# Kernel tuning notes

Measured on AMD Instinct MI355X. Metric: run time of the kernel, lower is better.

The kernel has to match this reference:

```python
import jax, jax.numpy as jnp
import numpy as np

B, N, H = 8, 1024, 256
ALPHA = 0.25


def setup_inputs() -> dict:
    key = jax.random.key(0)
    ks = jax.random.split(key, 10)
    h_cat = jax.random.normal(ks[0], (B, N, H), jnp.float32) * 0.1
    # Random trees: every node j>=1 gets a parent p in [0, j-1], on the left or right side.
    rng = np.random.default_rng(0)
    parents = (rng.random((B, N)) * np.arange(N)).astype(np.int64)  # parents[b,0] unused
    side = rng.integers(0, 2, (B, N))
    left = np.zeros((B, N, N), np.float32)
    right = np.zeros((B, N, N), np.float32)
    bidx = np.repeat(np.arange(B), N - 1)
    jidx = np.tile(np.arange(1, N), B)
    pidx = parents[:, 1:].reshape(-1)
    sid = side[:, 1:].reshape(-1)
    l = sid == 0
    r = sid == 1
    left[bidx[l], pidx[l], jidx[l]] = 1.0
    right[bidx[r], pidx[r], jidx[r]] = 1.0
    roots = jnp.zeros((B,), jnp.int32)  # node 0 is the root of each random tree
    return {
        "h_cat": h_cat,
        "left_adj": jnp.asarray(left),
        "right_adj": jnp.asarray(right),
        "roots": roots,
        "W_bilin": jax.random.normal(ks[1], (2, H, H), jnp.float32) * 0.02,
        "b_bilin": jax.random.normal(ks[2], (2,), jnp.float32) * 0.02,
        "W_head": jax.random.normal(ks[3], (2, H), jnp.float32) * 0.1,
        "W_dep": jax.random.normal(ks[4], (2, H), jnp.float32) * 0.1,
        "W_r1": jax.random.normal(ks[5], (H, H), jnp.float32) * 0.05,
        "b_r1": jnp.zeros((H,), jnp.float32),
        "W_r2": jax.random.normal(ks[6], (1, H), jnp.float32) * 0.1,
        "b_r2": jnp.zeros((1,), jnp.float32),
    }


def reference(h_cat, left_adj, right_adj, roots, W_bilin, b_bilin, W_head, W_dep, W_r1, b_r1, W_r2, b_r2):
    b, n, _ = h_cat.shape
    # --- biaffine compat matrix [b,n,n,2] (get_compat_matrix / bilin_compat),
    # computed via einsum instead of materializing the repeat_interleave [b,n*n,H] tensors.
    tmp = jnp.einsum('bih,khg->bikg', h_cat, W_bilin)          # [b,n,2,H]
    bil = jnp.einsum('bikg,bjg->bijk', tmp, h_cat)              # [b,n,n,2]
    head = h_cat @ W_head.T                                     # [b,n,2]
    dep = h_cat @ W_dep.T                                       # [b,n,2]
    compat = bil + head[:, :, None, :] + dep[:, None, :, :] + b_bilin
    # --- root classifier: Linear -> GELU(exact) -> Linear, [b,n]
    root_scores = (jax.nn.gelu(h_cat @ W_r1.T + b_r1, approximate=False) @ W_r2.T + b_r2)[..., 0]
    # --- logistic_loss (matrix-tree theorem)
    gold = root_scores[jnp.arange(b), roots]
    gold = gold + jnp.sum(compat[..., 0] * left_adj, axis=(1, 2))
    gold = gold + jnp.sum(compat[..., 1] * right_adj, axis=(1, 2))
    A = jnp.sum(jnp.exp(compat), axis=3)                        # [b,n,n]
    colsum = jnp.sum(A, axis=1)                                 # [b,n]
    lap = -A
    diag = jnp.arange(n)
    lap = lap.at[:, diag, diag].add(colsum)                     # diag_embed(sum(A,1)) - A
    lap = lap.at[:, 0, :].set(jnp.exp(root_scores))             # replace row 0 with root potentials
    sign, logabs = jnp.linalg.slogdet(lap)
    logdet = jnp.where(sign > 0, logabs, jnp.nan)               # torch logdet -> nan for det<=0
    valid = ((~jnp.isnan(gold)) & (~jnp.isnan(logdet))).astype(gold.dtype)
    mask = (gold <= logdet * valid).astype(gold.dtype)
    loss = (logdet - gold) * mask
    loss = jnp.where(jnp.isnan(loss), 0.0, loss)
    return ALPHA * jnp.sum(loss) / b
```

## Files before the change

kernel.cpp:

```cpp
#include <hip/hip_runtime.h>
#include <math.h>

#define BB 8
#define NN 1024
#define HH 256
#define ALPHAC 0.25f

typedef short bf16x8 __attribute__((ext_vector_type(8)));
typedef unsigned short u16x8 __attribute__((ext_vector_type(8)));
typedef float f32x4 __attribute__((ext_vector_type(4)));

__device__ inline unsigned short f2bf(float x) {
  unsigned u = __builtin_bit_cast(unsigned, x);
  unsigned r = (u + 0x7fffu + ((u >> 16) & 1u)) >> 16;
  return (unsigned short)r;
}
__device__ inline float bf2f(unsigned short u) {
  return __builtin_bit_cast(float, (unsigned)u << 16);
}

__device__ inline int prm(int i) { return i == 0 ? 1023 : (i == 1023 ? 0 : i); }

static const size_t OFF_TMPBF = 0;
static const size_t OFF_HBF   = 2097152;
static const size_t OFF_BT    = 3145728;
static const size_t OFF_EL    = 3244040;
static const size_t OFF_EV    = 3252240;
static const size_t OFF_R1    = 3260448;
static const size_t OFF_M     = 4325376;
static const size_t OFF_SM    = 8519680;
static const size_t O_H0 = 0, O_H1 = 8192, O_D0 = 16384, O_D1 = 24576, O_RS = 32768;
static const size_t O_GOLD = 40960, O_SLOG = 40968, O_NEG = 40976, O_ZER = 40984;
static const size_t O_CS   = 40992;

__global__ __launch_bounds__(256) void kA_pre(const float* __restrict__ h_cat,
    const float* __restrict__ Wb, const float* __restrict__ Wr1,
    const float* __restrict__ W_head, const float* __restrict__ W_dep,
    const float* __restrict__ left, const float* __restrict__ right,
    unsigned short* __restrict__ h_bf, unsigned short* __restrict__ BT,
    float* __restrict__ head0, float* __restrict__ head1,
    float* __restrict__ dep0, float* __restrict__ dep1,
    unsigned* __restrict__ par) {
  int bid = blockIdx.x, tid = threadIdx.x;
  if (bid < 2048) {
    int wave = tid >> 6, lane = tid & 63;
    int row = bid * 4 + wave;
    float4 h4 = *(const float4*)&h_cat[(size_t)row * 256 + lane * 4];
    ushort4 o;
    o.x = f2bf(h4.x); o.y = f2bf(h4.y); o.z = f2bf(h4.z); o.w = f2bf(h4.w);
    *(ushort4*)&h_bf[(size_t)row * 256 + lane * 4] = o;
    float4 wh0 = *(const float4*)&W_head[lane * 4];
    float4 wh1 = *(const float4*)&W_head[256 + lane * 4];
    float4 wd0 = *(const float4*)&W_dep[lane * 4];
    float4 wd1 = *(const float4*)&W_dep[256 + lane * 4];
    float s0 = h4.x * wh0.x + h4.y * wh0.y + h4.z * wh0.z + h4.w * wh0.w;
    float s1 = h4.x * wh1.x + h4.y * wh1.y + h4.z * wh1.z + h4.w * wh1.w;
    float s2 = h4.x * wd0.x + h4.y * wd0.y + h4.z * wd0.z + h4.w * wd0.w;
    float s3 = h4.x * wd1.x + h4.y * wd1.y + h4.z * wd1.z + h4.w * wd1.w;
#pragma unroll
    for (int off = 32; off; off >>= 1) {
      s0 += __shfl_down(s0, off);
      s1 += __shfl_down(s1, off);
      s2 += __shfl_down(s2, off);
      s3 += __shfl_down(s3, off);
    }
    if (lane == 0) {
      head0[row] = s0; head1[row] = s1; dep0[row] = s2; dep1[row] = s3;
    }
  } else if (bid < 2560) {
    int idx = (bid - 2048) * 256 + tid;
    int c = idx >> 8, h = idx & 255;
    BT[(size_t)c * 256 + h] = f2bf(Wb[(size_t)(c >> 8) * 65536 + (size_t)h * 256 + (c & 255)]);
  } else if (bid < 2816) {
    int idx = (bid - 2560) * 256 + tid;
    int c = idx >> 8, h = idx & 255;
    BT[(size_t)(512 + c) * 256 + h] = f2bf(Wr1[(size_t)c * 256 + h]);
  } else {
    int base = (bid - 2816) * 256 + tid;
#pragma unroll
    for (int it = 0; it < 2; ++it) {
      int g = base + it * 1048576;
      float4 v = *(const float4*)&left[(size_t)g * 4];
      if (v.x != 0.f || v.y != 0.f || v.z != 0.f || v.w != 0.f) {
        float va[4] = {v.x, v.y, v.z, v.w};
#pragma unroll
        for (int c = 0; c < 4; ++c)
          if (va[c] != 0.f) {
            int e = g * 4 + c;
            par[((e >> 20) << 10) | (e & 1023)] = (unsigned)((e >> 10) & 1023);
          }
      }
      float4 u = *(const float4*)&right[(size_t)g * 4];
      if (u.x != 0.f || u.y != 0.f || u.z != 0.f || u.w != 0.f) {
        float ua[4] = {u.x, u.y, u.z, u.w};
#pragma unroll
        for (int c = 0; c < 4; ++c)
          if (ua[c] != 0.f) {
            int e = g * 4 + c;
            par[((e >> 20) << 10) | (e & 1023)] = 0x80000000u | (unsigned)((e >> 10) & 1023);
          }
      }
    }
  }
}

__global__ __launch_bounds__(1024) void kF(const unsigned short* __restrict__ h_bf,
    const unsigned short* __restrict__ BT, const float* __restrict__ b_bilin,
    const float* __restrict__ head0, const float* __restrict__ head1,
    const float* __restrict__ dep0, const float* __restrict__ dep1,
    unsigned short* __restrict__ tmp_bf, unsigned short* __restrict__ r1pre,
    unsigned short* __restrict__ M, float* __restrict__ colsum) {
  __shared__ __align__(16) unsigned short tmpS[64][520];
  __shared__ __align__(16) unsigned short hA[64][264];
  int tid = threadIdx.x;
  int lane = tid & 63, w = tid >> 6;
  int fr = lane & 15, kof = (lane >> 4) * 8;
  int bid = blockIdx.x;
  int b = bid & 7;
  int n = bid >> 3;
  int it = n >> 1, jh = n & 1;
  int i0 = it * 64;
  size_t bN = (size_t)b * NN;
#pragma unroll
  for (int s = 0; s < 2; ++s) {
    int g = tid + s * 1024;
    int r = g >> 5, c8 = (g & 31) * 8;
    *(u16x8*)&hA[r][c8] = *(const u16x8*)&h_bf[(bN + i0 + r) * 256 + c8];
  }
  __syncthreads();
  {
    int c0 = w * 32;
    f32x4 acc[4][2] = {};
#pragma unroll
    for (int k = 0; k < 8; ++k) {
      bf16x8 a[4], bb[2];
#pragma unroll
      for (int rt = 0; rt < 4; ++rt)
        a[rt] = *(const bf16x8*)&hA[rt * 16 + fr][k * 32 + kof];
#pragma unroll
      for (int ct = 0; ct < 2; ++ct)
        bb[ct] = *(const bf16x8*)&BT[(size_t)(c0 + ct * 16 + fr) * 256 + k * 32 + kof];
#pragma unroll
      for (int rt = 0; rt < 4; ++rt)
#pragma unroll
        for (int ct = 0; ct < 2; ++ct)
          acc[rt][ct] = __builtin_amdgcn_mfma_f32_16x16x32_bf16(a[rt], bb[ct], acc[rt][ct], 0, 0, 0);
    }
#pragma unroll
    for (int rt = 0; rt < 4; ++rt)
#pragma unroll
      for (int ct = 0; ct < 2; ++ct)
#pragma unroll
        for (int q = 0; q < 4; ++q)
          tmpS[rt * 16 + (lane >> 4) * 4 + q][c0 + ct * 16 + fr] = f2bf(acc[rt][ct][q]);
  }
  if (jh == 0) {
    f32x4 accr[4] = {};
#pragma unroll
    for (int k = 0; k < 8; ++k) {
      bf16x8 br = *(const bf16x8*)&BT[(size_t)(512 + w * 16 + fr) * 256 + k * 32 + kof];
#pragma unroll
      for (int rt = 0; rt < 4; ++rt) {
        bf16x8 a = *(const bf16x8*)&hA[rt * 16 + fr][k * 32 + kof];
        accr[rt] = __builtin_amdgcn_mfma_f32_16x16x32_bf16(a, br, accr[rt], 0, 0, 0);
      }
    }
#pragma unroll
    for (int rt = 0; rt < 4; ++rt)
#pragma unroll
      for (int q = 0; q < 4; ++q)
        r1pre[(bN + i0 + rt * 16 + (lane >> 4) * 4 + q) * 256 + w * 16 + fr] = f2bf(accr[rt][q]);
  }
  __syncthreads();
  if (jh == 0) {
#pragma unroll
    for (int itc = 0; itc < 4; ++itc) {
      int g = tid + itc * 1024;
      int r = g >> 6, c8 = (g & 63) * 8;
      *(u16x8*)&tmp_bf[(bN + i0 + r) * 512 + c8] = *(const u16x8*)&tmpS[r][c8];
    }
  }
  int j0 = jh * 512 + w * 32;
  f32x4 acc0[4][2] = {}, acc1[4][2] = {};
#pragma unroll
  for (int k = 0; k < 8; ++k) {
    bf16x8 bfr[2];
#pragma unroll
    for (int ct = 0; ct < 2; ++ct)
      bfr[ct] = *(const bf16x8*)&h_bf[(bN + j0 + ct * 16 + fr) * 256 + k * 32 + kof];
#pragma unroll
    for (int rt = 0; rt < 4; ++rt) {
      bf16x8 a0 = *(const bf16x8*)&tmpS[rt * 16 + fr][k * 32 + kof];
      bf16x8 a1 = *(const bf16x8*)&tmpS[rt * 16 + fr][256 + k * 32 + kof];
#pragma unroll
      for (int ct = 0; ct < 2; ++ct) {
        acc0[rt][ct] = __builtin_amdgcn_mfma_f32_16x16x32_bf16(a0, bfr[ct], acc0[rt][ct], 0, 0, 0);
        acc1[rt][ct] = __builtin_amdgcn_mfma_f32_16x16x32_bf16(a1, bfr[ct], acc1[rt][ct], 0, 0, 0);
      }
    }
  }
  float bb0 = b_bilin[0], bb1 = b_bilin[1];
  float d0a[2], d1a[2];
#pragma unroll
  for (int ct = 0; ct < 2; ++ct) {
    int j = j0 + ct * 16 + fr;
    d0a[ct] = dep0[bN + j];
    d1a[ct] = dep1[bN + j];
  }
  unsigned short outv[4][2][4];
  float csum[2] = {};
#pragma unroll
  for (int rt = 0; rt < 4; ++rt)
#pragma unroll
    for (int q = 0; q < 4; ++q) {
      int i = i0 + rt * 16 + (lane >> 4) * 4 + q;
      float h0 = head0[bN + i], h1 = head1[bN + i];
#pragma unroll
      for (int ct = 0; ct < 2; ++ct) {
        float c0 = acc0[rt][ct][q] + h0 + d0a[ct] + bb0;
        float c1 = acc1[rt][ct][q] + h1 + d1a[ct] + bb1;
        float aexp = __expf(c0) + __expf(c1);
        csum[ct] += aexp;
        outv[rt][ct][q] = f2bf(-aexp);
      }
    }
#pragma unroll
  for (int ct = 0; ct < 2; ++ct) {
    float v = csum[ct];
    v += __shfl_down(v, 32);
    v += __shfl_down(v, 16);
    if (lane < 16) atomicAdd(&colsum[bN + prm(j0 + ct * 16 + lane)], v);
  }
  __syncthreads();
#pragma unroll
  for (int rt = 0; rt < 4; ++rt)
#pragma unroll
    for (int ct = 0; ct < 2; ++ct)
#pragma unroll
      for (int q = 0; q < 4; ++q)
        tmpS[rt * 16 + (lane >> 4) * 4 + q][w * 32 + ct * 16 + fr] = outv[rt][ct][q];
  __syncthreads();
  size_t Mb = (size_t)b * NN * NN;
#pragma unroll
  for (int itc = 0; itc < 4; ++itc) {
    int g = tid + itc * 1024;
    int r = g >> 6, c8 = (g & 63) * 8;
    int pi = prm(i0 + r);
    int j8 = jh * 512 + c8;
    if ((jh == 0 && c8 == 0) || (jh == 1 && c8 == 504)) {
#pragma unroll
      for (int u = 0; u < 8; ++u)
        M[Mb + (size_t)pi * NN + prm(j8 + u)] = tmpS[r][c8 + u];
    } else {
      *(u16x8*)&M[Mb + (size_t)pi * NN + j8] = *(const u16x8*)&tmpS[r][c8];
    }
  }
}

__global__ __launch_bounds__(256) void kB_post(const unsigned* __restrict__ par,
    const unsigned short* __restrict__ tmp_bf, const unsigned short* __restrict__ h_bf,
    const float* __restrict__ head0, const float* __restrict__ head1,
    const float* __restrict__ dep0, const float* __restrict__ dep1,
    const float* __restrict__ b_bilin, const unsigned short* __restrict__ r1pre,
    const float* __restrict__ b_r1, const float* __restrict__ W_r2,
    const float* __restrict__ b_r2, float* __restrict__ edgeval,
    float* __restrict__ rs) {
  int bid = blockIdx.x, tid = threadIdx.x;
  int w = tid >> 6, lane = tid & 63;
  if (bid < 2046) {
    int ei = bid * 4 + w;
    if (ei >= 8184) return;
    int b = ei / 1023;
    int j = ei - b * 1023 + 1;
    unsigned p = par[(b << 10) + j];
    int s = (int)(p >> 31);
    int i = (int)(p & 1023u);
    const unsigned short* tp = tmp_bf + (size_t)(b * NN + i) * 512 + s * 256 + lane * 4;
    const unsigned short* hp = h_bf + (size_t)(b * NN + j) * 256 + lane * 4;
    ushort4 tv = *(const ushort4*)tp;
    ushort4 hv = *(const ushort4*)hp;
    float dot = bf2f(tv.x) * bf2f(hv.x) + bf2f(tv.y) * bf2f(hv.y) +
                bf2f(tv.z) * bf2f(hv.z) + bf2f(tv.w) * bf2f(hv.w);
#pragma unroll
    for (int off = 32; off; off >>= 1) dot += __shfl_down(dot, off);
    if (lane == 0)
      edgeval[ei] = dot + (s ? head1 : head0)[b * NN + i] + (s ? dep1 : dep0)[b * NN + j] + b_bilin[s];
  } else if (bid < 4094) {
    int row = (bid - 2046) * 4 + w;
    ushort4 r4 = *(const ushort4*)&r1pre[(size_t)row * 256 + lane * 4];
    float4 br4 = *(const float4*)&b_r1[lane * 4];
    float4 wr2 = *(const float4*)&W_r2[lane * 4];
    float xa = bf2f(r4.x) + br4.x, xb = bf2f(r4.y) + br4.y;
    float xc = bf2f(r4.z) + br4.z, xd = bf2f(r4.w) + br4.w;
    float ga = 0.5f * xa * (1.0f + erff(xa * 0.70710678118654752f));
    float gb = 0.5f * xb * (1.0f + erff(xb * 0.70710678118654752f));
    float gc = 0.5f * xc * (1.0f + erff(xc * 0.70710678118654752f));
    float gd = 0.5f * xd * (1.0f + erff(xd * 0.70710678118654752f));
    float s4 = ga * wr2.x + gb * wr2.y + gc * wr2.z + gd * wr2.w;
#pragma unroll
    for (int off = 32; off; off >>= 1) s4 += __shfl_down(s4, off);
    if (lane == 0) rs[row] = s4 + b_r2[0];
  }
}

__global__ __launch_bounds__(1024) void k3b_diag(unsigned short* __restrict__ M,
    const float* __restrict__ colsum, const float* __restrict__ rs) {
  int j = threadIdx.x;
  int b = blockIdx.x;
  unsigned short* Mb = M + (size_t)b * NN * NN;
  float d = bf2f(Mb[(size_t)j * NN + j]) + colsum[b * NN + j];
  if (j != 1023) Mb[(size_t)j * NN + j] = f2bf(d);
  Mb[(size_t)1023 * NN + j] = f2bf(expf(rs[b * NN + prm(j)]));
}

#define AS(r, c) sb[(r) * 72 + (c)]
#define CSS(r, c) sb[(r) * 136 + (c)]
__global__ __launch_bounds__(256) void k6_schur256(unsigned short* __restrict__ M, int k0,
    int nt_c, float* __restrict__ slog, int* __restrict__ negc, int* __restrict__ zerc) {
  __shared__ __align__(16) unsigned short sb[4608 + 128 * 72];
  __shared__ float rd[256];
  int tid = threadIdx.x;
  int bid = blockIdx.x;
  int b = bid & 7;
  int n = bid >> 3;
  int by = n / nt_c, bx = n - by * nt_c;
  unsigned short* Mb = M + (size_t)b * NN * NN;
  {
    float d = bf2f(Mb[(size_t)(k0 + tid) * NN + k0 + tid]);
    rd[tid] = 1.0f / d;
    if (n == 0) {
      float lf = logf(fabsf(d));
      int flg = (d < 0.f ? 1 : 0) + (d == 0.f ? (1 << 16) : 0);
#pragma unroll
      for (int off = 32; off; off >>= 1) { lf += __shfl_down(lf, off); flg += __shfl_down(flg, off); }
      if ((tid & 63) == 0) { atomicAdd(&slog[b], lf); atomicAdd(&negc[b], flg & 0xffff); atomicAdd(&zerc[b], flg >> 16); }
    }
  }
  int i0 = k0 + 256 + by * 64;
  int j0 = k0 + 256 + bx * 128;
  int lane = tid & 63, w = tid >> 6;
  int rb = w * 16, fr = lane & 15, kof = (lane >> 4) * 8, cb = lane & 15;
  f32x4 acc[8] = {};
#pragma unroll
  for (int kc = 0; kc < 4; ++kc) {
    __syncthreads();
#pragma unroll
    for (int it = 0; it < 4; ++it) {
      int g = tid + it * 256;
      if (it < 2) {
        int r = g >> 3, c = (g & 7) * 8;
        u16x8 vv = *(const u16x8*)&Mb[(size_t)(i0 + r) * NN + k0 + kc * 64 + c];
        u16x8 ov;
#pragma unroll
        for (int u = 0; u < 8; ++u) ov[u] = f2bf(bf2f(vv[u]) * rd[kc * 64 + c + u]);
        *(u16x8*)&AS(r, c) = ov;
      }
      int r2 = g >> 4, c2 = (g & 15) * 8;
      u16x8 uu = *(const u16x8*)&Mb[(size_t)(k0 + kc * 64 + r2) * NN + j0 + c2];
#pragma unroll
      for (int u = 0; u < 8; ++u) {
        int col = c2 + u;
        sb[4608 + col * 72 + ((((r2 >> 3) ^ ((col >> 3) & 7)) << 3) | (r2 & 7))] = uu[u];
      }
    }
    __syncthreads();
#pragma unroll
    for (int ks = 0; ks < 2; ++ks) {
      bf16x8 a = *(const bf16x8*)&AS(rb + fr, ks * 32 + kof);
      int G = (ks * 32 + kof) >> 3;
#pragma unroll
      for (int t = 0; t < 8; ++t) {
        int R = t * 16 + fr;
        bf16x8 bb = *(const bf16x8*)&sb[4608 + R * 72 + ((G ^ ((R >> 3) & 7)) << 3)];
        acc[t] = __builtin_amdgcn_mfma_f32_16x16x32_bf16(a, bb, acc[t], 0, 0, 0);
      }
    }
  }
  __syncthreads();
  {
    int rr = rb + (lane >> 4) * 4;
#pragma unroll
    for (int t = 0; t < 8; ++t)
#pragma unroll
      for (int q = 0; q < 4; ++q) CSS(rr + q, t * 16 + cb) = f2bf(acc[t][q]);
  }
  __syncthreads();
#pragma unroll
  for (int it = 0; it < 4; ++it) {
    int g = it * 256 + tid;
    int r = g >> 4, c8 = (g & 15) * 8;
    unsigned short* gp = &Mb[(size_t)(i0 + r) * NN + j0 + c8];
    u16x8 old = *(const u16x8*)gp;
    u16x8 del = *(const u16x8*)&CSS(r, c8);
    u16x8 out;
#pragma unroll
    for (int u = 0; u < 8; ++u) out[u] = f2bf(bf2f(old[u]) - bf2f(del[u]));
    *(u16x8*)gp = out;
  }
}

__global__ __launch_bounds__(1024) void k9_final(const unsigned short* __restrict__ M,
    float* __restrict__ slog, int* __restrict__ negc, int* __restrict__ zerc) {
  __shared__ __align__(16) unsigned short As[128][136];
  __shared__ __align__(16) unsigned short Bt[128 * 136];
  __shared__ float Cs[128][132];
  __shared__ float rdv[128];
  __shared__ float wsum[16];
  __shared__ int wflg[16];
  int b = blockIdx.x, tid = threadIdx.x;
  int lane = tid & 63, w = tid >> 6;
  const unsigned short* Mb = M + (size_t)b * NN * NN;
  float lfacc = 0.f; int flacc = 0;
  if (tid < 128) {
    float d = bf2f(Mb[(size_t)(768 + tid) * NN + 768 + tid]);
    rdv[tid] = 1.0f / d;
    lfacc += logf(fabsf(d));
    flacc += (d < 0.f ? 1 : 0) + (d == 0.f ? (1 << 16) : 0);
  }
  __syncthreads();
#pragma unroll
  for (int it = 0; it < 2; ++it) {
    int g = tid + it * 1024;
    int r = g >> 4, c8 = (g & 15) * 8;
    u16x8 vv = *(const u16x8*)&Mb[(size_t)(896 + r) * NN + 768 + c8];
    u16x8 ov;
#pragma unroll
    for (int u = 0; u < 8; ++u) ov[u] = f2bf(bf2f(vv[u]) * rdv[c8 + u]);
    *(u16x8*)&As[r][c8] = ov;
    u16x8 uu = *(const u16x8*)&Mb[(size_t)(768 + r) * NN + 896 + c8];
    int X = ((r >> 3) ^ (c8 >> 3)) & 15;
    int pb = c8 * 136 + X * 8 + (r & 7);
#pragma unroll
    for (int u = 0; u < 8; ++u) Bt[pb + u * 136] = uu[u];
    u16x8 cc = *(const u16x8*)&Mb[(size_t)(896 + r) * NN + 896 + c8];
#pragma unroll
    for (int u = 0; u < 8; ++u) Cs[r][c8 + u] = bf2f(cc[u]);
  }
  __syncthreads();
  {
    int tr = w >> 1, cg = w & 1;
    int rb = tr * 16, fr = lane & 15, kof = (lane >> 4) * 8, cb = lane & 15;
    f32x4 acc[4] = {};
#pragma unroll
    for (int kc = 0; kc < 4; ++kc) {
      bf16x8 a = *(const bf16x8*)&As[rb + fr][kof + kc * 32];
      int K8 = (kc * 32 + kof) >> 3;
#pragma unroll
      for (int t = 0; t < 4; ++t) {
        int c = cg * 64 + t * 16 + fr;
        bf16x8 bb = *(const bf16x8*)&Bt[c * 136 + ((K8 ^ ((c >> 3) & 15)) << 3)];
        acc[t] = __builtin_amdgcn_mfma_f32_16x16x32_bf16(a, bb, acc[t], 0, 0, 0);
      }
    }
#pragma unroll
    for (int t = 0; t < 4; ++t)
#pragma unroll
      for (int q = 0; q < 4; ++q)
        Cs[rb + (lane >> 4) * 4 + q][cg * 64 + t * 16 + cb] -= acc[t][q];
  }
  __syncthreads();
  if (tid < 64) {
    float d = Cs[tid][tid];
    rdv[tid] = 1.0f / d;
    lfacc += logf(fabsf(d));
    flacc += (d < 0.f ? 1 : 0) + (d == 0.f ? (1 << 16) : 0);
  }
  __syncthreads();
  {
    int ty = tid >> 5, tx = tid & 31;
    float acc[2][2] = {};
    for (int k = 0; k < 64; ++k) {
      float ik = rdv[k];
      float a0 = Cs[64 + ty * 2 + 0][k] * ik;
      float a1 = Cs[64 + ty * 2 + 1][k] * ik;
      float b0 = Cs[k][64 + tx * 2 + 0];
      float b1 = Cs[k][64 + tx * 2 + 1];
      acc[0][0] += a0 * b0; acc[0][1] += a0 * b1;
      acc[1][0] += a1 * b0; acc[1][1] += a1 * b1;
    }
#pragma unroll
    for (int r = 0; r < 2; ++r)
#pragma unroll
      for (int c = 0; c < 2; ++c)
        Cs[64 + ty * 2 + r][64 + tx * 2 + c] -= acc[r][c];
  }
  __syncthreads();
  if (tid < 32) {
    float d = Cs[64 + tid][64 + tid];
    rdv[tid] = 1.0f / d;
    lfacc += logf(fabsf(d));
    flacc += (d < 0.f ? 1 : 0) + (d == 0.f ? (1 << 16) : 0);
  }
  __syncthreads();
  {
    int r = tid >> 5, c = tid & 31;
    float acc = 0.f;
    for (int k = 0; k < 32; ++k)
      acc += Cs[96 + r][64 + k] * rdv[k] * Cs[64 + k][96 + c];
    Cs[96 + r][96 + c] -= acc;
  }
  __syncthreads();
  {
    int r5 = tid >> 3, c4 = (tid & 7) * 4;
    for (int j = 0; j < 31; ++j) {
      if (tid < 256 && r5 > j) {
        float inv = 1.0f / Cs[96 + j][96 + j];
        float lrj = Cs[96 + r5][96 + j] * inv;
#pragma unroll
        for (int u = 0; u < 4; ++u) {
          int c = c4 + u;
          if (c > j) Cs[96 + r5][96 + c] -= lrj * Cs[96 + j][96 + c];
        }
      }
      __syncthreads();
    }
    if (tid < 32) {
      float d = Cs[96 + tid][96 + tid];
      lfacc += logf(fabsf(d));
      flacc += (d < 0.f ? 1 : 0) + (d == 0.f ? (1 << 16) : 0);
    }
  }
#pragma unroll
  for (int off = 32; off; off >>= 1) { lfacc += __shfl_down(lfacc, off); flacc += __shfl_down(flacc, off); }
  if (lane == 0) { wsum[w] = lfacc; wflg[w] = flacc; }
  __syncthreads();
  if (tid == 0) {
    float lf = 0.f; int fl = 0;
#pragma unroll
    for (int i = 0; i < 16; ++i) { lf += wsum[i]; fl += wflg[i]; }
    atomicAdd(&slog[b], lf);
    atomicAdd(&negc[b], fl & 0xffff);
    atomicAdd(&zerc[b], fl >> 16);
  }
}

__global__ __launch_bounds__(512) void k7_final(const float* __restrict__ edgeval,
    const float* __restrict__ rs, const int* __restrict__ roots,
    const float* __restrict__ slog, const int* __restrict__ negc,
    const int* __restrict__ zerc, float* __restrict__ out) {
  __shared__ float gld[8];
  int w = threadIdx.x >> 6, lane = threadIdx.x & 63;
  float s = 0.f;
  for (int e = lane; e < 1023; e += 64) s += edgeval[w * 1023 + e];
#pragma unroll
  for (int off = 32; off; off >>= 1) s += __shfl_down(s, off);
  if (lane == 0) gld[w] = s;
  __syncthreads();
  if (threadIdx.x == 0) {
    float acc = 0.f;
    for (int b = 0; b < BB; ++b) {
      int root = roots[b];
      float gold = rs[b * NN + root] + gld[b];
      float ld = slog[b];
      bool pos = ((negc[b] & 1) == 0) && (zerc[b] == 0);
      float loss = 0.f;
      if (pos && !isnan(ld) && !isnan(gold)) {
        if (gold <= ld) loss = ld - gold;
      }
      if (isnan(loss) || isinf(loss)) loss = 0.f;
      acc += loss;
    }
    out[0] = ALPHAC * acc / (float)BB;
  }
}

extern "C" void kernel_launch(void* const* d_in, const int* in_sizes, int n_in,
                              void* d_out, int out_size, void* d_ws, size_t ws_size,
                              hipStream_t stream) {
  (void)in_sizes; (void)n_in; (void)out_size; (void)ws_size;
  const float* h_cat  = (const float*)d_in[0];
  const float* left   = (const float*)d_in[1];
  const float* right  = (const float*)d_in[2];
  const int*   roots  = (const int*)d_in[3];
  const float* W_bilin = (const float*)d_in[4];
  const float* b_bilin = (const float*)d_in[5];
  const float* W_head = (const float*)d_in[6];
  const float* W_dep  = (const float*)d_in[7];
  const float* W_r1   = (const float*)d_in[8];
  const float* b_r1   = (const float*)d_in[9];
  const float* W_r2   = (const float*)d_in[10];
  const float* b_r2   = (const float*)d_in[11];

  float* ws = (float*)d_ws;
  unsigned short* tmp_bf = (unsigned short*)(ws + OFF_TMPBF);
  unsigned short* h_bf   = (unsigned short*)(ws + OFF_HBF);
  unsigned short* BT     = (unsigned short*)(ws + OFF_BT);
  unsigned* par  = (unsigned*)(ws + OFF_EL);
  float* edgeval = ws + OFF_EV;
  unsigned short* r1pre  = (unsigned short*)(ws + OFF_R1);
  unsigned short* M = (unsigned short*)(ws + OFF_M);
  float* sm    = ws + OFF_SM;
  float* head0 = sm + O_H0;
  float* head1 = sm + O_H1;
  float* dep0  = sm + O_D0;
  float* dep1  = sm + O_D1;
  float* rs    = sm + O_RS;
  float* gold  = sm + O_GOLD;
  float* slog  = sm + O_SLOG;
  int*   negc  = (int*)(sm + O_NEG);
  int*   zerc  = (int*)(sm + O_ZER);
  float* colsum = sm + O_CS;

  hipMemsetAsync(gold, 0, (32 + BB * NN) * sizeof(float), stream);

  kA_pre<<<6912, 256, 0, stream>>>(h_cat, W_bilin, W_r1, W_head, W_dep, left, right,
                                   h_bf, BT, head0, head1, dep0, dep1, par);
  kF<<<256, 1024, 0, stream>>>(h_bf, BT, b_bilin, head0, head1, dep0, dep1,
                               tmp_bf, r1pre, M, colsum);
  kB_post<<<4094, 256, 0, stream>>>(par, tmp_bf, h_bf, head0, head1, dep0, dep1,
                                    b_bilin, r1pre, b_r1, W_r2, b_r2, edgeval, rs);
  k3b_diag<<<8, 1024, 0, stream>>>(M, colsum, rs);
  for (int s = 0; s < 3; ++s) {
    int k0 = s * 256;
    int rem = 1024 - 256 - k0;
    int nt_r = rem / 64, nt_c = rem / 128;
    k6_schur256<<<nt_r * nt_c * 8, 256, 0, stream>>>(M, k0, nt_c, slog, negc, zerc);
  }
  k9_final<<<8, 1024, 0, stream>>>(M, slog, negc, zerc);
  k7_final<<<1, 512, 0, stream>>>(edgeval, rs, roots, slog, negc, zerc, (float*)d_out);
}
```

Measured before the change: 122.8 us.

## Retile kF to 32-row blocks covering all columns, dropping redundant tmp recompute

kF previously used 64-row i-tiles split into two column halves, so each half recomputed the same h·W_bilin tmp product. It now gives each block 32 rows and all 1024 columns, computing tmp once per row tile and writing both column halves of M through shared memory in two passes. The aim is to remove the duplicated first GEMM and keep the block count unchanged. In exchange each block does more sequential work, holds more accumulators per thread, and the h_bf B-fragment loads are no longer shared across as many rows.

Result: slower. 128.9 us (+5.0%).

```diff
diff --git a/kernel.cpp b/kernel.cpp
--- a/kernel.cpp
+++ b/kernel.cpp
@@ -110,149 +110,153 @@
     const float* __restrict__ dep0, const float* __restrict__ dep1,
     unsigned short* __restrict__ tmp_bf, unsigned short* __restrict__ r1pre,
     unsigned short* __restrict__ M, float* __restrict__ colsum) {
-  __shared__ __align__(16) unsigned short tmpS[64][520];
-  __shared__ __align__(16) unsigned short hA[64][264];
+  __shared__ __align__(16) unsigned short tmpS[32][520];
+  __shared__ __align__(16) unsigned short hA[32][264];
   int tid = threadIdx.x;
   int lane = tid & 63, w = tid >> 6;
   int fr = lane & 15, kof = (lane >> 4) * 8;
   int bid = blockIdx.x;
   int b = bid & 7;
-  int n = bid >> 3;
-  int it = n >> 1, jh = n & 1;
-  int i0 = it * 64;
+  int it = bid >> 3;
+  int i0 = it * 32;
   size_t bN = (size_t)b * NN;
-#pragma unroll
-  for (int s = 0; s < 2; ++s) {
-    int g = tid + s * 1024;
-    int r = g >> 5, c8 = (g & 31) * 8;
+  {
+    int r = tid >> 5, c8 = (tid & 31) * 8;
     *(u16x8*)&hA[r][c8] = *(const u16x8*)&h_bf[(bN + i0 + r) * 256 + c8];
   }
   __syncthreads();
   {
     int c0 = w * 32;
-    f32x4 acc[4][2] = {};
+    f32x4 acc[2][2] = {};
 #pragma unroll
     for (int k = 0; k < 8; ++k) {
-      bf16x8 a[4], bb[2];
-#pragma unroll
-      for (int rt = 0; rt < 4; ++rt)
+      bf16x8 a[2], bb[2];
+#pragma unroll
+      for (int rt = 0; rt < 2; ++rt)
         a[rt] = *(const bf16x8*)&hA[rt * 16 + fr][k * 32 + kof];
 #pragma unroll
       for (int ct = 0; ct < 2; ++ct)
         bb[ct] = *(const bf16x8*)&BT[(size_t)(c0 + ct * 16 + fr) * 256 + k * 32 + kof];
 #pragma unroll
-      for (int rt = 0; rt < 4; ++rt)
+      for (int rt = 0; rt < 2; ++rt)
 #pragma unroll
         for (int ct = 0; ct < 2; ++ct)
           acc[rt][ct] = __builtin_amdgcn_mfma_f32_16x16x32_bf16(a[rt], bb[ct], acc[rt][ct], 0, 0, 0);
     }
 #pragma unroll
-    for (int rt = 0; rt < 4; ++rt)
+    for (int rt = 0; rt < 2; ++rt)
 #pragma unroll
       for (int ct = 0; ct < 2; ++ct)
 #pragma unroll
         for (int q = 0; q < 4; ++q)
           tmpS[rt * 16 + (lane >> 4) * 4 + q][c0 + ct * 16 + fr] = f2bf(acc[rt][ct][q]);
   }
-  if (jh == 0) {
-    f32x4 accr[4] = {};
+  {
+    f32x4 accr[2] = {};
 #pragma unroll
     for (int k = 0; k < 8; ++k) {
       bf16x8 br = *(const bf16x8*)&BT[(size_t)(512 + w * 16 + fr) * 256 + k * 32 + kof];
 #pragma unroll
-      for (int rt = 0; rt < 4; ++rt) {
+      for (int rt = 0; rt < 2; ++rt) {
         bf16x8 a = *(const bf16x8*)&hA[rt * 16 + fr][k * 32 + kof];
         accr[rt] = __builtin_amdgcn_mfma_f32_16x16x32_bf16(a, br, accr[rt], 0, 0, 0);
       }
     }
 #pragma unroll
-    for (int rt = 0; rt < 4; ++rt)
+    for (int rt = 0; rt < 2; ++rt)
 #pragma unroll
       for (int q = 0; q < 4; ++q)
         r1pre[(bN + i0 + rt * 16 + (lane >> 4) * 4 + q) * 256 + w * 16 + fr] = f2bf(accr[rt][q]);
   }
   __syncthreads();
-  if (jh == 0) {
-#pragma unroll
-    for (int itc = 0; itc < 4; ++itc) {
+#pragma unroll
+  for (int itc = 0; itc < 2; ++itc) {
+    int g = tid + itc * 1024;
+    int r = g >> 6, c8 = (g & 63) * 8;
+    *(u16x8*)&tmp_bf[(bN + i0 + r) * 512 + c8] = *(const u16x8*)&tmpS[r][c8];
+  }
+  f32x4 acc0[2][2][2] = {}, acc1[2][2][2] = {};
+#pragma unroll
+  for (int k = 0; k < 8; ++k) {
+    bf16x8 bfr[2][2];
+#pragma unroll
+    for (int hf = 0; hf < 2; ++hf)
+#pragma unroll
+      for (int ct = 0; ct < 2; ++ct)
+        bfr[hf][ct] = *(const bf16x8*)&h_bf[(bN + hf * 512 + w * 32 + ct * 16 + fr) * 256 + k * 32 + kof];
+#pragma unroll
+    for (int rt = 0; rt < 2; ++rt) {
+      bf16x8 a0 = *(const bf16x8*)&tmpS[rt * 16 + fr][k * 32 + kof];
+      bf16x8 a1 = *(const bf16x8*)&tmpS[rt * 16 + fr][256 + k * 32 + kof];
+#pragma unroll
+      for (int hf = 0; hf < 2; ++hf)
+#pragma unroll
+        for (int ct = 0; ct < 2; ++ct) {
+          acc0[hf][rt][ct] = __builtin_amdgcn_mfma_f32_16x16x32_bf16(a0, bfr[hf][ct], acc0[hf][rt][ct], 0, 0, 0);
+          acc1[hf][rt][ct] = __builtin_amdgcn_mfma_f32_16x16x32_bf16(a1, bfr[hf][ct], acc1[hf][rt][ct], 0, 0, 0);
+        }
+    }
+  }
+  float bb0 = b_bilin[0], bb1 = b_bilin[1];
+  size_t Mb = (size_t)b * NN * NN;
+  unsigned short outv[2][2][2][4];
+#pragma unroll
+  for (int hf = 0; hf < 2; ++hf) {
+    float d0a[2], d1a[2];
+#pragma unroll
+    for (int ct = 0; ct < 2; ++ct) {
+      int j = hf * 512 + w * 32 + ct * 16 + fr;
+      d0a[ct] = dep0[bN + j];
+      d1a[ct] = dep1[bN + j];
+    }
+    float csum[2] = {};
+#pragma unroll
+    for (int rt = 0; rt < 2; ++rt)
+#pragma unroll
+      for (int q = 0; q < 4; ++q) {
+        int i = i0 + rt * 16 + (lane >> 4) * 4 + q;
+        float h0 = head0[bN + i], h1 = head1[bN + i];
+#pragma unroll
+        for (int ct = 0; ct < 2; ++ct) {
+          float c0 = acc0[hf][rt][ct][q] + h0 + d0a[ct] + bb0;
+          float c1 = acc1[hf][rt][ct][q] + h1 + d1a[ct] + bb1;
+          float aexp = __expf(c0) + __expf(c1);
+          csum[ct] += aexp;
+          outv[hf][rt][ct][q] = f2bf(-aexp);
+        }
+      }
+#pragma unroll
+    for (int ct = 0; ct < 2; ++ct) {
+      float v = csum[ct];
+      v += __shfl_down(v, 32);
+      v += __shfl_down(v, 16);
+      if (lane < 16) atomicAdd(&colsum[bN + prm(hf * 512 + w * 32 + ct * 16 + lane)], v);
+    }
+  }
+#pragma unroll
+  for (int hf = 0; hf < 2; ++hf) {
+    __syncthreads();
+#pragma unroll
+    for (int rt = 0; rt < 2; ++rt)
+#pragma unroll
+      for (int ct = 0; ct < 2; ++ct)
+#pragma unroll
+        for (int q = 0; q < 4; ++q)
+          tmpS[rt * 16 + (lane >> 4) * 4 + q][w * 32 + ct * 16 + fr] = outv[hf][rt][ct][q];
+    __syncthreads();
+#pragma unroll
+    for (int itc = 0; itc < 2; ++itc) {
       int g = tid + itc * 1024;
       int r = g >> 6, c8 = (g & 63) * 8;
-      *(u16x8*)&tmp_bf[(bN + i0 + r) * 512 + c8] = *(const u16x8*)&tmpS[r][c8];
-    }
-  }
-  int j0 = jh * 512 + w * 32;
-  f32x4 acc0[4][2] = {}, acc1[4][2] = {};
-#pragma unroll
-  for (int k = 0; k < 8; ++k) {
-    bf16x8 bfr[2];
-#pragma unroll
-    for (int ct = 0; ct < 2; ++ct)
-      bfr[ct] = *(const bf16x8*)&h_bf[(bN + j0 + ct * 16 + fr) * 256 + k * 32 + kof];
-#pragma unroll
-    for (int rt = 0; rt < 4; ++rt) {
-      bf16x8 a0 = *(const bf16x8*)&tmpS[rt * 16 + fr][k * 32 + kof];
-      bf16x8 a1 = *(const bf16x8*)&tmpS[rt * 16 + fr][256 + k * 32 + kof];
-#pragma unroll
-      for (int ct = 0; ct < 2; ++ct) {
-        acc0[rt][ct] = __builtin_amdgcn_mfma_f32_16x16x32_bf16(a0, bfr[ct], acc0[rt][ct], 0, 0, 0);
-        acc1[rt][ct] = __builtin_amdgcn_mfma_f32_16x16x32_bf16(a1, bfr[ct], acc1[rt][ct], 0, 0, 0);
-      }
-    }
-  }
-  float bb0 = b_bilin[0], bb1 = b_bilin[1];
-  float d0a[2], d1a[2];
-#pragma unroll
-  for (int ct = 0; ct < 2; ++ct) {
-    int j = j0 + ct * 16 + fr;
-    d0a[ct] = dep0[bN + j];
-    d1a[ct] = dep1[bN + j];
-  }
-  unsigned short outv[4][2][4];
-  float csum[2] = {};
-#pragma unroll
-  for (int rt = 0; rt < 4; ++rt)
-#pragma unroll
-    for (int q = 0; q < 4; ++q) {
-      int i = i0 + rt * 16 + (lane >> 4) * 4 + q;
-      float h0 = head0[bN + i], h1 = head1[bN + i];
-#pragma unroll
-      for (int ct = 0; ct < 2; ++ct) {
-        float c0 = acc0[rt][ct][q] + h0 + d0a[ct] + bb0;
-        float c1 = acc1[rt][ct][q] + h1 + d1a[ct] + bb1;
-        float aexp = __expf(c0) + __expf(c1);
-        csum[ct] += aexp;
-        outv[rt][ct][q] = f2bf(-aexp);
-      }
-    }
-#pragma unroll
-  for (int ct = 0; ct < 2; ++ct) {
-    float v = csum[ct];
-    v += __shfl_down(v, 32);
-    v += __shfl_down(v, 16);
-    if (lane < 16) atomicAdd(&colsum[bN + prm(j0 + ct * 16 + lane)], v);
-  }
-  __syncthreads();
-#pragma unroll
-  for (int rt = 0; rt < 4; ++rt)
-#pragma unroll
-    for (int ct = 0; ct < 2; ++ct)
-#pragma unroll
-      for (int q = 0; q < 4; ++q)
-        tmpS[rt * 16 + (lane >> 4) * 4 + q][w * 32 + ct * 16 + fr] = outv[rt][ct][q];
-  __syncthreads();
-  size_t Mb = (size_t)b * NN * NN;
-#pragma unroll
-  for (int itc = 0; itc < 4; ++itc) {
-    int g = tid + itc * 1024;
-    int r = g >> 6, c8 = (g & 63) * 8;
-    int pi = prm(i0 + r);
-    int j8 = jh * 512 + c8;
-    if ((jh == 0 && c8 == 0) || (jh == 1 && c8 == 504)) {
-#pragma unroll
-      for (int u = 0; u < 8; ++u)
-        M[Mb + (size_t)pi * NN + prm(j8 + u)] = tmpS[r][c8 + u];
-    } else {
-      *(u16x8*)&M[Mb + (size_t)pi * NN + j8] = *(const u16x8*)&tmpS[r][c8];
+      int pi = prm(i0 + r);
+      int j8 = hf * 512 + c8;
+      if ((hf == 0 && c8 == 0) || (hf == 1 && c8 == 504)) {
+#pragma unroll
+        for (int u = 0; u < 8; ++u)
+          M[Mb + (size_t)pi * NN + prm(j8 + u)] = tmpS[r][c8 + u];
+      } else {
+        *(u16x8*)&M[Mb + (size_t)pi * NN + j8] = *(const u16x8*)&tmpS[r][c8];
+      }
     }
   }
 }
```
